# Kernel optimization log

Hardware: AMD Instinct MI355X
Metric: run time of the kernel (lower is better)

## Reference

```python
import jax, jax.numpy as jnp
import numpy as np
import math

D_MODEL, D_K, D_V, H = 512, 64, 64, 8

def setup_inputs() -> dict:
    key = jax.random.key(0)
    ks = jax.random.split(key, 8)
    B, L = 2, 4096
    q = jax.random.normal(ks[0], (B, L, D_MODEL), dtype=jnp.float32)
    k = jax.random.normal(ks[1], (B, L, D_MODEL), dtype=jnp.float32)
    v = jax.random.normal(ks[2], (B, L, D_MODEL), dtype=jnp.float32)
    attention_mask = jnp.ones((B, L), dtype=jnp.int32)
    s = 1.0 / math.sqrt(D_MODEL)
    Wq = jax.random.uniform(ks[3], (D_MODEL, H * D_K), dtype=jnp.float32, minval=-s, maxval=s)
    Wk = jax.random.uniform(ks[4], (D_MODEL, H * D_K), dtype=jnp.float32, minval=-s, maxval=s)
    Wv = jax.random.uniform(ks[5], (D_MODEL, H * D_V), dtype=jnp.float32, minval=-s, maxval=s)
    so = 1.0 / math.sqrt(H * D_V)
    Wo = jax.random.uniform(ks[6], (H * D_V, D_MODEL), dtype=jnp.float32, minval=-so, maxval=so)
    return {"q": q, "k": k, "v": v, "attention_mask": attention_mask,
            "Wq": Wq, "Wk": Wk, "Wv": Wv, "Wo": Wo}

def reference(q, k, v, attention_mask, Wq, Wk, Wv, Wo):
    B, L, _ = q.shape
    scale = 1.0 / math.sqrt(D_K)
    # project and split heads: [B, H, L, d]
    qh = (q @ Wq).reshape(B, L, H, D_K).transpose(0, 2, 1, 3)
    kh = (k @ Wk).reshape(B, L, H, D_K).transpose(0, 2, 1, 3)
    vh = (v @ Wv).reshape(B, L, H, D_V).transpose(0, 2, 1, 3)
    score = jnp.einsum('bhqd,bhkd->bhqk', qh, kh) * scale  # [B,H,L,L]
    mask = attention_mask[:, None, None, :]  # [B,1,1,L]
    score = jnp.where(mask == 0, -jnp.inf, score)
    attn = jax.nn.softmax(score, axis=-1)
    out = jnp.einsum('bhqk,bhkd->bhqd', attn, vh)
    out = out.transpose(0, 2, 1, 3).reshape(B, L, H * D_V)
    return out @ Wo
```

## Files before the change

### kernel.cpp

```cpp
#include <hip/hip_runtime.h>

typedef short bf16x8 __attribute__((ext_vector_type(8)));
typedef float f32x4 __attribute__((ext_vector_type(4)));
typedef unsigned short u16x8 __attribute__((ext_vector_type(8)));

static __device__ __forceinline__ unsigned short f2bf(float f) {
  unsigned int x = __builtin_bit_cast(unsigned int, f);
  x += 0x7FFFu + ((x >> 16) & 1u);
  return (unsigned short)(x >> 16);
}
static __device__ __forceinline__ unsigned int pk2bf(float a, float b) {
  unsigned int ia = __builtin_bit_cast(unsigned int, a) + 0x8000u;
  unsigned int ib = __builtin_bit_cast(unsigned int, b) + 0x8000u;
  return __builtin_amdgcn_perm(ib, ia, 0x07060302u);
}
static __device__ __forceinline__ void gl2lds16(const unsigned short* g, unsigned short* l) {
  __builtin_amdgcn_global_load_lds(
      (const __attribute__((address_space(1))) unsigned int*)g,
      (__attribute__((address_space(3))) unsigned int*)l, 16, 0, 0);
}

__global__ __launch_bounds__(256) void cvt3(const float* __restrict__ q, const float* __restrict__ k,
                                            const float* __restrict__ v,
                                            unsigned short* __restrict__ xbf) {
  const int sec = blockIdx.y;
  const float* src = (sec == 0) ? q : (sec == 1) ? k : v;
  int i = (blockIdx.x * 256 + threadIdx.x) * 8;
  int row = i >> 9, col = i & 511;
  float4 a = *(const float4*)(src + i);
  float4 b = *(const float4*)(src + i + 4);
  uint4 pk;
  pk.x = pk2bf(a.x, a.y); pk.y = pk2bf(a.z, a.w);
  pk.z = pk2bf(b.x, b.y); pk.w = pk2bf(b.z, b.w);
  *(uint4*)(xbf + (size_t)row * 1536 + sec * 512 + col) = pk;
}

__global__ __launch_bounds__(256) void wtrans4(const float* __restrict__ Wq, const float* __restrict__ Wk,
                                               const float* __restrict__ Wv, const float* __restrict__ Wo,
                                               unsigned short* __restrict__ WT) {
  __shared__ __align__(16) float T[64 * 68];
  const int z = blockIdx.z;
  const float* W = (z == 0) ? Wq : (z == 1) ? Wk : (z == 2) ? Wv : Wo;
  unsigned short* out = WT + (size_t)z * 512 * 512;
  const int k0 = blockIdx.x * 64, n0 = blockIdx.y * 64;
  const int tid = threadIdx.x;
#pragma unroll
  for (int i = 0; i < 4; ++i) {
    int chunk = i * 256 + tid;
    int row = chunk >> 4, fc = chunk & 15;
    *(float4*)(T + row * 68 + fc * 4) =
        *(const float4*)(W + (size_t)(k0 + row) * 512 + n0 + fc * 4);
  }
  __syncthreads();
#pragma unroll
  for (int i = 0; i < 2; ++i) {
    int chunk = i * 256 + tid;
    int nr = chunk >> 3, kc = chunk & 7;
    u16x8 v;
#pragma unroll
    for (int j = 0; j < 8; ++j) v[j] = f2bf(T[(kc * 8 + j) * 68 + nr]);
    *(u16x8*)(out + (size_t)(n0 + nr) * 512 + k0 + kc * 8) = v;
  }
}

__global__ __launch_bounds__(256) void gemm_qkv(const unsigned short* __restrict__ xbf,
                                                const unsigned short* __restrict__ Bt,
                                                unsigned short* __restrict__ C,
                                                float qscale) {
  __shared__ __align__(16) unsigned short Abuf[2][128 * 32];
  __shared__ __align__(16) unsigned short Bbuf[2][128 * 32];
  const int by = blockIdx.y;
  const unsigned short* A = xbf + (by >> 2) * 512;
  const float scale = (by < 4) ? qscale : 1.0f;
  const int tid = threadIdx.x;
  const int wid = tid >> 6, lane = tid & 63, quad = lane >> 4, li = lane & 15;
  const int bm = blockIdx.x * 128, bn = by * 128;
  const int wm = (wid & 1) * 64, wn = (wid >> 1) * 64;
  const unsigned short* ga[2]; int oa[2];
  const unsigned short* gb[2]; int obx[2];
#pragma unroll
  for (int i = 0; i < 2; ++i) {
    int lam = i * 256 + tid;
    int r = lam >> 2, c = (lam & 3) ^ (r & 3);
    ga[i] = A + (size_t)(bm + r) * 1536 + c * 8;
    oa[i] = lam * 8;
    gb[i] = Bt + (size_t)(bn + r) * 512 + c * 8;
    obx[i] = lam * 8;
  }
#pragma unroll
  for (int i = 0; i < 2; ++i) {
    gl2lds16(ga[i], &Abuf[0][oa[i]]); ga[i] += 32;
    gl2lds16(gb[i], &Bbuf[0][obx[i]]); gb[i] += 32;
  }
  f32x4 acc[4][4] = {};
  const int sw = li & 3;
  for (int s = 0; s < 16; ++s) {
    __syncthreads();
    if (s + 1 < 16) {
      int p = (s + 1) & 1;
#pragma unroll
      for (int i = 0; i < 2; ++i) {
        gl2lds16(ga[i], &Abuf[p][oa[i]]); ga[i] += 32;
        gl2lds16(gb[i], &Bbuf[p][obx[i]]); gb[i] += 32;
      }
    }
    const unsigned short* As = &Abuf[s & 1][0];
    const unsigned short* Bs = &Bbuf[s & 1][0];
    bf16x8 af[4], bfr[4];
#pragma unroll
    for (int t = 0; t < 4; ++t) {
      af[t]  = *(const bf16x8*)(As + (wm + t * 16 + li) * 32 + ((quad ^ sw) * 8));
      bfr[t] = *(const bf16x8*)(Bs + (wn + t * 16 + li) * 32 + ((quad ^ sw) * 8));
    }
#pragma unroll
    for (int mt = 0; mt < 4; ++mt)
#pragma unroll
      for (int nt = 0; nt < 4; ++nt)
        acc[mt][nt] = __builtin_amdgcn_mfma_f32_16x16x32_bf16(af[mt], bfr[nt], acc[mt][nt], 0, 0, 0);
  }
#pragma unroll
  for (int mt = 0; mt < 4; ++mt)
#pragma unroll
    for (int nt = 0; nt < 4; ++nt) {
      int r0 = bm + wm + mt * 16 + quad * 4;
      int c  = bn + wn + nt * 16 + li;
#pragma unroll
      for (int r = 0; r < 4; ++r)
        C[(size_t)(r0 + r) * 1536 + c] = f2bf(acc[mt][nt][r] * scale);
    }
}

__global__ __launch_bounds__(256) void gemm_o(const unsigned short* __restrict__ A,
                                              const unsigned short* __restrict__ Bt,
                                              float* __restrict__ Cf) {
  __shared__ __align__(16) unsigned short Abuf[2][128 * 64];
  __shared__ __align__(16) unsigned short Bbuf[2][64 * 64];
  const int K = 512, LDC = 512;
  const int tid = threadIdx.x;
  const int wid = tid >> 6, lane = tid & 63, quad = lane >> 4, li = lane & 15;
  const int bm = blockIdx.x * 128, bn = blockIdx.y * 64;
  const int wm = wid * 32;
  const unsigned short* ga[4]; int oa[4];
  const unsigned short* gb[2]; int ob[2];
#pragma unroll
  for (int i = 0; i < 4; ++i) {
    int lam = i * 256 + wid * 64 + lane;
    int r = lam >> 3, c = (lam & 7) ^ (r & 7);
    ga[i] = A + (size_t)(bm + r) * K + c * 8;
    oa[i] = lam * 8;
  }
#pragma unroll
  for (int i = 0; i < 2; ++i) {
    int lam = i * 256 + wid * 64 + lane;
    int r = lam >> 3, c = (lam & 7) ^ (r & 7);
    gb[i] = Bt + (size_t)(bn + r) * K + c * 8;
    ob[i] = lam * 8;
  }
#pragma unroll
  for (int i = 0; i < 4; ++i) { gl2lds16(ga[i], &Abuf[0][oa[i]]); ga[i] += 64; }
#pragma unroll
  for (int i = 0; i < 2; ++i) { gl2lds16(gb[i], &Bbuf[0][ob[i]]); gb[i] += 64; }

  f32x4 acc[2][4] = {};
  const int sw = li & 7;
  for (int s = 0; s < 8; ++s) {
    __syncthreads();
    if (s + 1 < 8) {
      int p = (s + 1) & 1;
#pragma unroll
      for (int i = 0; i < 4; ++i) { gl2lds16(ga[i], &Abuf[p][oa[i]]); ga[i] += 64; }
#pragma unroll
      for (int i = 0; i < 2; ++i) { gl2lds16(gb[i], &Bbuf[p][ob[i]]); gb[i] += 64; }
    }
    const unsigned short* As = &Abuf[s & 1][0];
    const unsigned short* Bs = &Bbuf[s & 1][0];
#pragma unroll
    for (int kk = 0; kk < 2; ++kk) {
      bf16x8 af[2], bfr[4];
#pragma unroll
      for (int t = 0; t < 2; ++t)
        af[t] = *(const bf16x8*)(As + (wm + t * 16 + li) * 64 + (((kk * 4 + quad) ^ sw) * 8));
#pragma unroll
      for (int t = 0; t < 4; ++t)
        bfr[t] = *(const bf16x8*)(Bs + (t * 16 + li) * 64 + (((kk * 4 + quad) ^ sw) * 8));
#pragma unroll
      for (int mt = 0; mt < 2; ++mt)
#pragma unroll
        for (int nt = 0; nt < 4; ++nt)
          acc[mt][nt] = __builtin_amdgcn_mfma_f32_16x16x32_bf16(af[mt], bfr[nt], acc[mt][nt], 0, 0, 0);
    }
  }
#pragma unroll
  for (int mt = 0; mt < 2; ++mt)
#pragma unroll
    for (int nt = 0; nt < 4; ++nt) {
      int r0 = bm + wm + mt * 16 + quad * 4;
      int c  = bn + nt * 16 + li;
#pragma unroll
      for (int r = 0; r < 4; ++r)
        Cf[(size_t)(r0 + r) * LDC + c] = acc[mt][nt][r];
    }
}

__global__ __launch_bounds__(256) void vtrans(const unsigned short* __restrict__ qkv,
                                              unsigned short* __restrict__ vt) {
  __shared__ __align__(16) unsigned short T[64 * 72];
  const int kt = blockIdx.x;
  const int bh = blockIdx.y;
  const int b = bh >> 3, h = bh & 7;
  const int tid = threadIdx.x;
#pragma unroll
  for (int i = 0; i < 2; ++i) {
    int chunk = i * 256 + tid;
    int row = chunk >> 3, c8 = chunk & 7;
    *(uint4*)(T + row * 72 + c8 * 8) =
        *(const uint4*)(qkv + (size_t)(b * 4096 + kt * 64 + row) * 1536 + 1024 + h * 64 + c8 * 8);
  }
  __syncthreads();
#pragma unroll
  for (int i = 0; i < 2; ++i) {
    int chunk = i * 256 + tid;
    int dr = chunk >> 3, c8 = chunk & 7;
    u16x8 v;
#pragma unroll
    for (int j = 0; j < 8; ++j) v[j] = T[(c8 * 8 + j) * 72 + dr];
    *(u16x8*)(vt + (size_t)(bh * 64 + dr) * 4096 + kt * 64 + c8 * 8) = v;
  }
}

__global__ __launch_bounds__(512) void attn(const unsigned short* __restrict__ qkv,
                                            const unsigned short* __restrict__ vt,
                                            const int* __restrict__ mask,
                                            float* __restrict__ O0, float* __restrict__ O1,
                                            float* __restrict__ Lb) {
  __shared__ __align__(16) unsigned short Kbuf[2][64 * 64];
  __shared__ __align__(16) unsigned short Vbuf[2][64 * 64];
  __shared__ __align__(16) unsigned short Psh[8][16 * 72];
  __shared__ __align__(16) unsigned short MskBits[256];
  const int qt = blockIdx.x, h = blockIdx.y, z = blockIdx.z;
  const int b = z >> 1, half = z & 1;
  const int t0 = half * 32;
  const int tid = threadIdx.x;
  const int wid = tid >> 6, lane = tid & 63, quad = lane >> 4, li = lane & 15;
  const size_t tok0 = (size_t)b * 4096;

  if (tid < 256) {
    const int4* mp = (const int4*)(mask + b * 4096 + tid * 16);
    unsigned int bits = 0;
#pragma unroll
    for (int j = 0; j < 4; ++j) {
      int4 m4 = mp[j];
      bits |= (m4.x ? 1u : 0u) << (j * 4 + 0);
      bits |= (m4.y ? 1u : 0u) << (j * 4 + 1);
      bits |= (m4.z ? 1u : 0u) << (j * 4 + 2);
      bits |= (m4.w ? 1u : 0u) << (j * 4 + 3);
    }
    MskBits[tid] = (unsigned short)bits;
  }

  const unsigned short* qp = qkv + (tok0 + qt * 128 + wid * 16 + li) * 1536 + h * 64;
  bf16x8 bq0 = *(const bf16x8*)(qp + quad * 8);
  bf16x8 bq1 = *(const bf16x8*)(qp + 32 + quad * 8);

  const unsigned short* kbase = qkv + tok0 * 1536 + 512 + h * 64;
  const unsigned short* vbase = vt + (size_t)(b * 8 + h) * 64 * 4096;
  const int wk = wid & 3;
  const int lam0 = wk * 128 + lane, lam1 = lam0 + 64;
  const int r0 = lam0 >> 3, c0 = (lam0 & 7) ^ (r0 & 7);
  const int r1 = lam1 >> 3, c1 = (lam1 & 7) ^ (r1 & 7);
  const unsigned short *g0, *g1;
  size_t kstride;
  unsigned short *lb0, *lb1;
  if (wid < 4) {
    g0 = kbase + (size_t)(t0 * 64 + r0) * 1536 + c0 * 8;
    g1 = kbase + (size_t)(t0 * 64 + r1) * 1536 + c1 * 8;
    kstride = (size_t)64 * 1536;
    lb0 = &Kbuf[0][0]; lb1 = &Kbuf[1][0];
  } else {
    g0 = vbase + (size_t)r0 * 4096 + t0 * 64 + c0 * 8;
    g1 = vbase + (size_t)r1 * 4096 + t0 * 64 + c1 * 8;
    kstride = 64;
    lb0 = &Vbuf[0][0]; lb1 = &Vbuf[1][0];
  }
  const int o0 = lam0 * 8, o1 = lam1 * 8;

  gl2lds16(g0, lb0 + o0);
  gl2lds16(g1, lb0 + o1);
  g0 += kstride; g1 += kstride;

  f32x4 accO[4] = {};
  f32x4 accL = {};
  bf16x8 bones;
#pragma unroll
  for (int j = 0; j < 8; ++j) bones[j] = (short)0x3F80;
  unsigned short* Pw = &Psh[wid][0];
  const int sw = li & 7;

  for (int tt = 0; tt < 32; ++tt) {
    const int t = t0 + tt;
    __syncthreads();
    if (tt < 31) {
      unsigned short* lb = ((tt + 1) & 1) ? lb1 : lb0;
      gl2lds16(g0, lb + o0);
      gl2lds16(g1, lb + o1);
      g0 += kstride; g1 += kstride;
    }
    const unsigned short* Ks = &Kbuf[tt & 1][0];
    const unsigned short* Vs = &Vbuf[tt & 1][0];

    f32x4 s[4];
#pragma unroll
    for (int kb = 0; kb < 4; ++kb) {
      const unsigned short* kr = Ks + (kb * 16 + li) * 64;
      bf16x8 ak0 = *(const bf16x8*)(kr + ((quad ^ sw) * 8));
      bf16x8 ak1 = *(const bf16x8*)(kr + (((4 + quad) ^ sw) * 8));
      f32x4 zv = {};
      zv = __builtin_amdgcn_mfma_f32_16x16x32_bf16(ak0, bq0, zv, 0, 0, 0);
      zv = __builtin_amdgcn_mfma_f32_16x16x32_bf16(ak1, bq1, zv, 0, 0, 0);
      s[kb] = zv;
    }
    unsigned long long mbits = *(const unsigned long long*)(MskBits + t * 4);
    if (mbits != ~0ull) {
#pragma unroll
      for (int kb = 0; kb < 4; ++kb)
#pragma unroll
        for (int r = 0; r < 4; ++r) {
          int key = kb * 16 + quad * 4 + r;
          if (!((mbits >> key) & 1ull)) s[kb][r] = -1e30f;
        }
    }
#pragma unroll
    for (int kb = 0; kb < 4; ++kb) {
#pragma unroll
      for (int r = 0; r < 4; ++r) s[kb][r] = __builtin_amdgcn_exp2f(s[kb][r]);
      uint2 pk;
      pk.x = pk2bf(s[kb][0], s[kb][1]);
      pk.y = pk2bf(s[kb][2], s[kb][3]);
      *(uint2*)(Pw + li * 72 + kb * 16 + quad * 4) = pk;
    }
    bf16x8 p0 = *(const bf16x8*)(Pw + li * 72 + quad * 8);
    bf16x8 p1 = *(const bf16x8*)(Pw + li * 72 + 32 + quad * 8);
#pragma unroll
    for (int dc = 0; dc < 4; ++dc) {
      const unsigned short* vr = Vs + (dc * 16 + li) * 64;
      bf16x8 bv0 = *(const bf16x8*)(vr + ((quad ^ sw) * 8));
      bf16x8 bv1 = *(const bf16x8*)(vr + (((4 + quad) ^ sw) * 8));
      accO[dc] = __builtin_amdgcn_mfma_f32_16x16x32_bf16(p0, bv0, accO[dc], 0, 0, 0);
      accO[dc] = __builtin_amdgcn_mfma_f32_16x16x32_bf16(p1, bv1, accO[dc], 0, 0, 0);
    }
    accL = __builtin_amdgcn_mfma_f32_16x16x32_bf16(p0, bones, accL, 0, 0, 0);
    accL = __builtin_amdgcn_mfma_f32_16x16x32_bf16(p1, bones, accL, 0, 0, 0);
  }
  float* Oh = half ? O1 : O0;
  const size_t rq = tok0 + qt * 128 + wid * 16 + quad * 4;
#pragma unroll
  for (int dc = 0; dc < 4; ++dc) {
    size_t col = h * 64 + dc * 16 + li;
#pragma unroll
    for (int r = 0; r < 4; ++r)
      Oh[(rq + r) * 512 + col] = accO[dc][r];
  }
  if (li == 0) {
#pragma unroll
    for (int r = 0; r < 4; ++r)
      Lb[((size_t)half * 8192 + rq + r) * 8 + h] = accL[r];
  }
}

__global__ __launch_bounds__(256) void cmb(const float* __restrict__ O0, const float* __restrict__ O1,
                                           const float* __restrict__ Lb,
                                           unsigned short* __restrict__ ob) {
  int idx = (blockIdx.x * 256 + threadIdx.x) * 4;
  int tok = idx >> 9, h = (idx >> 6) & 7;
  float inv = 1.f / (Lb[(size_t)tok * 8 + h] + Lb[(size_t)(8192 + tok) * 8 + h]);
  float4 a = *(const float4*)(O0 + idx);
  float4 b = *(const float4*)(O1 + idx);
  uint2 pk;
  pk.x = pk2bf((a.x + b.x) * inv, (a.y + b.y) * inv);
  pk.y = pk2bf((a.z + b.z) * inv, (a.w + b.w) * inv);
  *(uint2*)(ob + idx) = pk;
}

extern "C" void kernel_launch(void* const* d_in, const int* in_sizes, int n_in,
                              void* d_out, int out_size, void* d_ws, size_t ws_size,
                              hipStream_t stream) {
  const float* q  = (const float*)d_in[0];
  const float* k  = (const float*)d_in[1];
  const float* v  = (const float*)d_in[2];
  const int* mask = (const int*)d_in[3];
  const float* Wq = (const float*)d_in[4];
  const float* Wk = (const float*)d_in[5];
  const float* Wv = (const float*)d_in[6];
  const float* Wo = (const float*)d_in[7];
  float* out = (float*)d_out;

  char* ws = (char*)d_ws;
  const size_t MB = 1024 * 1024;
  unsigned short* xbf  = (unsigned short*)(ws);
  unsigned short* vtb  = (unsigned short*)(ws + 16 * MB);
  unsigned short* obb  = (unsigned short*)(ws + 16 * MB);
  unsigned short* qkvh = (unsigned short*)(ws + 24 * MB);
  unsigned short* wAll = (unsigned short*)(ws + 48 * MB);
  unsigned short* woT  = wAll + (size_t)3 * 512 * 512;
  float* O0f = (float*)(ws);
  float* O1f = (float*)(ws + 50 * MB);
  float* Lb  = (float*)(ws + 66 * MB);

  dim3 cg(2048, 3);
  cvt3<<<cg, 256, 0, stream>>>(q, k, v, xbf);
  dim3 wg(8, 8, 4);
  wtrans4<<<wg, 256, 0, stream>>>(Wq, Wk, Wv, Wo, wAll);
  const float qscale = 0.125f * 1.44269504f;
  dim3 gq(64, 12);
  gemm_qkv<<<gq, 256, 0, stream>>>(xbf, wAll, qkvh, qscale);
  dim3 vg(64, 16);
  vtrans<<<vg, 256, 0, stream>>>(qkvh, vtb);
  dim3 ag(32, 8, 4);
  attn<<<ag, 512, 0, stream>>>(qkvh, vtb, mask, O0f, O1f, Lb);
  cmb<<<4096, 256, 0, stream>>>(O0f, O1f, Lb, obb);
  dim3 go(64, 8);
  gemm_o<<<go, 256, 0, stream>>>(obb, woT, out);
}
```

Baseline: 235.1 us.

## Fuse input conversion into QKV GEMM, combine into O GEMM, widen attention waves

Removes the separate fp32-to-bf16 conversion kernel by having the QKV GEMM load fp32 inputs through registers, convert them and store to LDS with software prefetch. Removes the split-combine kernel by folding normalization and the two-half sum into the output GEMM's A-tile load. Attention now uses 256 threads with each wave handling 32 query rows, so K/V tiles in LDS are reused across two MFMA row groups. Grid axes are swapped so blocks sharing the same A rows run adjacently. This trades async global-to-LDS loads for register-staged loads and more VGPR pressure in exchange for fewer launches and less intermediate memory traffic.

Result: slower. 287.7 us (+22.4%).

```diff
diff --git a/kernel.cpp b/kernel.cpp
--- a/kernel.cpp
+++ b/kernel.cpp
@@ -14,25 +14,16 @@
   unsigned int ib = __builtin_bit_cast(unsigned int, b) + 0x8000u;
   return __builtin_amdgcn_perm(ib, ia, 0x07060302u);
 }
+static __device__ __forceinline__ uint4 pk8bf(float4 a, float4 b) {
+  uint4 r;
+  r.x = pk2bf(a.x, a.y); r.y = pk2bf(a.z, a.w);
+  r.z = pk2bf(b.x, b.y); r.w = pk2bf(b.z, b.w);
+  return r;
+}
 static __device__ __forceinline__ void gl2lds16(const unsigned short* g, unsigned short* l) {
   __builtin_amdgcn_global_load_lds(
       (const __attribute__((address_space(1))) unsigned int*)g,
       (__attribute__((address_space(3))) unsigned int*)l, 16, 0, 0);
-}
-
-__global__ __launch_bounds__(256) void cvt3(const float* __restrict__ q, const float* __restrict__ k,
-                                            const float* __restrict__ v,
-                                            unsigned short* __restrict__ xbf) {
-  const int sec = blockIdx.y;
-  const float* src = (sec == 0) ? q : (sec == 1) ? k : v;
-  int i = (blockIdx.x * 256 + threadIdx.x) * 8;
-  int row = i >> 9, col = i & 511;
-  float4 a = *(const float4*)(src + i);
-  float4 b = *(const float4*)(src + i + 4);
-  uint4 pk;
-  pk.x = pk2bf(a.x, a.y); pk.y = pk2bf(a.z, a.w);
-  pk.z = pk2bf(b.x, b.y); pk.w = pk2bf(b.z, b.w);
-  *(uint4*)(xbf + (size_t)row * 1536 + sec * 512 + col) = pk;
 }
 
 __global__ __launch_bounds__(256) void wtrans4(const float* __restrict__ Wq, const float* __restrict__ Wk,
@@ -63,45 +54,61 @@
   }
 }
 
-__global__ __launch_bounds__(256) void gemm_qkv(const unsigned short* __restrict__ xbf,
+__global__ __launch_bounds__(256) void gemm_qkv(const float* __restrict__ Aq, const float* __restrict__ Ak,
+                                                const float* __restrict__ Av,
                                                 const unsigned short* __restrict__ Bt,
-                                                unsigned short* __restrict__ C,
-                                                float qscale) {
+                                                unsigned short* __restrict__ C, float qscale) {
   __shared__ __align__(16) unsigned short Abuf[2][128 * 32];
   __shared__ __align__(16) unsigned short Bbuf[2][128 * 32];
-  const int by = blockIdx.y;
-  const unsigned short* A = xbf + (by >> 2) * 512;
+  const int by = blockIdx.x;
+  const float* A = (by < 4) ? Aq : (by < 8) ? Ak : Av;
   const float scale = (by < 4) ? qscale : 1.0f;
   const int tid = threadIdx.x;
   const int wid = tid >> 6, lane = tid & 63, quad = lane >> 4, li = lane & 15;
-  const int bm = blockIdx.x * 128, bn = by * 128;
+  const int bm = blockIdx.y * 128, bn = by * 128;
   const int wm = (wid & 1) * 64, wn = (wid >> 1) * 64;
-  const unsigned short* ga[2]; int oa[2];
   const unsigned short* gb[2]; int obx[2];
 #pragma unroll
   for (int i = 0; i < 2; ++i) {
     int lam = i * 256 + tid;
-    int r = lam >> 2, c = (lam & 3) ^ (r & 3);
-    ga[i] = A + (size_t)(bm + r) * 1536 + c * 8;
-    oa[i] = lam * 8;
-    gb[i] = Bt + (size_t)(bn + r) * 512 + c * 8;
+    int r = lam >> 2, cc = (lam & 3) ^ (r & 3);
+    gb[i] = Bt + (size_t)(bn + r) * 512 + cc * 8;
     obx[i] = lam * 8;
   }
-#pragma unroll
-  for (int i = 0; i < 2; ++i) {
-    gl2lds16(ga[i], &Abuf[0][oa[i]]); ga[i] += 32;
-    gl2lds16(gb[i], &Bbuf[0][obx[i]]); gb[i] += 32;
-  }
+  int ar[2], ac[2], ao[2];
+#pragma unroll
+  for (int i = 0; i < 2; ++i) {
+    int c = i * 256 + tid;
+    ar[i] = c >> 2;
+    ac[i] = ((c & 3) ^ (ar[i] & 3)) * 8;
+    ao[i] = c * 8;
+  }
+  float4 av0[2], av1[2];
+#pragma unroll
+  for (int i = 0; i < 2; ++i) {
+    const float* ap = A + (size_t)(bm + ar[i]) * 512 + ac[i];
+    av0[i] = *(const float4*)ap;
+    av1[i] = *(const float4*)(ap + 4);
+  }
+#pragma unroll
+  for (int i = 0; i < 2; ++i) *(uint4*)(&Abuf[0][ao[i]]) = pk8bf(av0[i], av1[i]);
+#pragma unroll
+  for (int i = 0; i < 2; ++i) { gl2lds16(gb[i], &Bbuf[0][obx[i]]); gb[i] += 32; }
+
   f32x4 acc[4][4] = {};
   const int sw = li & 3;
   for (int s = 0; s < 16; ++s) {
     __syncthreads();
-    if (s + 1 < 16) {
-      int p = (s + 1) & 1;
+    const bool pf = (s + 1 < 16);
+    const int p = (s + 1) & 1;
+    if (pf) {
+#pragma unroll
+      for (int i = 0; i < 2; ++i) { gl2lds16(gb[i], &Bbuf[p][obx[i]]); gb[i] += 32; }
 #pragma unroll
       for (int i = 0; i < 2; ++i) {
-        gl2lds16(ga[i], &Abuf[p][oa[i]]); ga[i] += 32;
-        gl2lds16(gb[i], &Bbuf[p][obx[i]]); gb[i] += 32;
+        const float* ap = A + (size_t)(bm + ar[i]) * 512 + (s + 1) * 32 + ac[i];
+        av0[i] = *(const float4*)ap;
+        av1[i] = *(const float4*)(ap + 4);
       }
     }
     const unsigned short* As = &Abuf[s & 1][0];
@@ -117,6 +124,10 @@
 #pragma unroll
       for (int nt = 0; nt < 4; ++nt)
         acc[mt][nt] = __builtin_amdgcn_mfma_f32_16x16x32_bf16(af[mt], bfr[nt], acc[mt][nt], 0, 0, 0);
+    if (pf) {
+#pragma unroll
+      for (int i = 0; i < 2; ++i) *(uint4*)(&Abuf[p][ao[i]]) = pk8bf(av0[i], av1[i]);
+    }
   }
 #pragma unroll
   for (int mt = 0; mt < 4; ++mt)
@@ -127,78 +138,6 @@
 #pragma unroll
       for (int r = 0; r < 4; ++r)
         C[(size_t)(r0 + r) * 1536 + c] = f2bf(acc[mt][nt][r] * scale);
-    }
-}
-
-__global__ __launch_bounds__(256) void gemm_o(const unsigned short* __restrict__ A,
-                                              const unsigned short* __restrict__ Bt,
-                                              float* __restrict__ Cf) {
-  __shared__ __align__(16) unsigned short Abuf[2][128 * 64];
-  __shared__ __align__(16) unsigned short Bbuf[2][64 * 64];
-  const int K = 512, LDC = 512;
-  const int tid = threadIdx.x;
-  const int wid = tid >> 6, lane = tid & 63, quad = lane >> 4, li = lane & 15;
-  const int bm = blockIdx.x * 128, bn = blockIdx.y * 64;
-  const int wm = wid * 32;
-  const unsigned short* ga[4]; int oa[4];
-  const unsigned short* gb[2]; int ob[2];
-#pragma unroll
-  for (int i = 0; i < 4; ++i) {
-    int lam = i * 256 + wid * 64 + lane;
-    int r = lam >> 3, c = (lam & 7) ^ (r & 7);
-    ga[i] = A + (size_t)(bm + r) * K + c * 8;
-    oa[i] = lam * 8;
-  }
-#pragma unroll
-  for (int i = 0; i < 2; ++i) {
-    int lam = i * 256 + wid * 64 + lane;
-    int r = lam >> 3, c = (lam & 7) ^ (r & 7);
-    gb[i] = Bt + (size_t)(bn + r) * K + c * 8;
-    ob[i] = lam * 8;
-  }
-#pragma unroll
-  for (int i = 0; i < 4; ++i) { gl2lds16(ga[i], &Abuf[0][oa[i]]); ga[i] += 64; }
-#pragma unroll
-  for (int i = 0; i < 2; ++i) { gl2lds16(gb[i], &Bbuf[0][ob[i]]); gb[i] += 64; }
-
-  f32x4 acc[2][4] = {};
-  const int sw = li & 7;
-  for (int s = 0; s < 8; ++s) {
-    __syncthreads();
-    if (s + 1 < 8) {
-      int p = (s + 1) & 1;
-#pragma unroll
-      for (int i = 0; i < 4; ++i) { gl2lds16(ga[i], &Abuf[p][oa[i]]); ga[i] += 64; }
-#pragma unroll
-      for (int i = 0; i < 2; ++i) { gl2lds16(gb[i], &Bbuf[p][ob[i]]); gb[i] += 64; }
-    }
-    const unsigned short* As = &Abuf[s & 1][0];
-    const unsigned short* Bs = &Bbuf[s & 1][0];
-#pragma unroll
-    for (int kk = 0; kk < 2; ++kk) {
-      bf16x8 af[2], bfr[4];
-#pragma unroll
-      for (int t = 0; t < 2; ++t)
-        af[t] = *(const bf16x8*)(As + (wm + t * 16 + li) * 64 + (((kk * 4 + quad) ^ sw) * 8));
-#pragma unroll
-      for (int t = 0; t < 4; ++t)
-        bfr[t] = *(const bf16x8*)(Bs + (t * 16 + li) * 64 + (((kk * 4 + quad) ^ sw) * 8));
-#pragma unroll
-      for (int mt = 0; mt < 2; ++mt)
-#pragma unroll
-        for (int nt = 0; nt < 4; ++nt)
-          acc[mt][nt] = __builtin_amdgcn_mfma_f32_16x16x32_bf16(af[mt], bfr[nt], acc[mt][nt], 0, 0, 0);
-    }
-  }
-#pragma unroll
-  for (int mt = 0; mt < 2; ++mt)
-#pragma unroll
-    for (int nt = 0; nt < 4; ++nt) {
-      int r0 = bm + wm + mt * 16 + quad * 4;
-      int c  = bn + nt * 16 + li;
-#pragma unroll
-      for (int r = 0; r < 4; ++r)
-        Cf[(size_t)(r0 + r) * LDC + c] = acc[mt][nt][r];
     }
 }
 
@@ -228,14 +167,14 @@
   }
 }
 
-__global__ __launch_bounds__(512) void attn(const unsigned short* __restrict__ qkv,
+__global__ __launch_bounds__(256) void attn(const unsigned short* __restrict__ qkv,
                                             const unsigned short* __restrict__ vt,
                                             const int* __restrict__ mask,
                                             float* __restrict__ O0, float* __restrict__ O1,
                                             float* __restrict__ Lb) {
   __shared__ __align__(16) unsigned short Kbuf[2][64 * 64];
   __shared__ __align__(16) unsigned short Vbuf[2][64 * 64];
-  __shared__ __align__(16) unsigned short Psh[8][16 * 72];
+  __shared__ __align__(16) unsigned short Psh[4][32 * 72];
   __shared__ __align__(16) unsigned short MskBits[256];
   const int qt = blockIdx.x, h = blockIdx.y, z = blockIdx.z;
   const int b = z >> 1, half = z & 1;
@@ -244,7 +183,7 @@
   const int wid = tid >> 6, lane = tid & 63, quad = lane >> 4, li = lane & 15;
   const size_t tok0 = (size_t)b * 4096;
 
-  if (tid < 256) {
+  {
     const int4* mp = (const int4*)(mask + b * 4096 + tid * 16);
     unsigned int bits = 0;
 #pragma unroll
@@ -258,38 +197,34 @@
     MskBits[tid] = (unsigned short)bits;
   }
 
-  const unsigned short* qp = qkv + (tok0 + qt * 128 + wid * 16 + li) * 1536 + h * 64;
-  bf16x8 bq0 = *(const bf16x8*)(qp + quad * 8);
-  bf16x8 bq1 = *(const bf16x8*)(qp + 32 + quad * 8);
+  const unsigned short* qpa = qkv + (tok0 + qt * 128 + wid * 32 + li) * 1536 + h * 64;
+  const unsigned short* qpb = qpa + 16 * 1536;
+  bf16x8 bq0a = *(const bf16x8*)(qpa + quad * 8);
+  bf16x8 bq1a = *(const bf16x8*)(qpa + 32 + quad * 8);
+  bf16x8 bq0b = *(const bf16x8*)(qpb + quad * 8);
+  bf16x8 bq1b = *(const bf16x8*)(qpb + 32 + quad * 8);
 
   const unsigned short* kbase = qkv + tok0 * 1536 + 512 + h * 64;
   const unsigned short* vbase = vt + (size_t)(b * 8 + h) * 64 * 4096;
-  const int wk = wid & 3;
-  const int lam0 = wk * 128 + lane, lam1 = lam0 + 64;
-  const int r0 = lam0 >> 3, c0 = (lam0 & 7) ^ (r0 & 7);
-  const int r1 = lam1 >> 3, c1 = (lam1 & 7) ^ (r1 & 7);
-  const unsigned short *g0, *g1;
-  size_t kstride;
-  unsigned short *lb0, *lb1;
-  if (wid < 4) {
-    g0 = kbase + (size_t)(t0 * 64 + r0) * 1536 + c0 * 8;
-    g1 = kbase + (size_t)(t0 * 64 + r1) * 1536 + c1 * 8;
-    kstride = (size_t)64 * 1536;
-    lb0 = &Kbuf[0][0]; lb1 = &Kbuf[1][0];
-  } else {
-    g0 = vbase + (size_t)r0 * 4096 + t0 * 64 + c0 * 8;
-    g1 = vbase + (size_t)r1 * 4096 + t0 * 64 + c1 * 8;
-    kstride = 64;
-    lb0 = &Vbuf[0][0]; lb1 = &Vbuf[1][0];
-  }
-  const int o0 = lam0 * 8, o1 = lam1 * 8;
-
-  gl2lds16(g0, lb0 + o0);
-  gl2lds16(g1, lb0 + o1);
-  g0 += kstride; g1 += kstride;
-
-  f32x4 accO[4] = {};
-  f32x4 accL = {};
+  const unsigned short *gk[2], *gv[2];
+  int okc[2], ovc[2];
+#pragma unroll
+  for (int i = 0; i < 2; ++i) {
+    int c = i * 256 + tid;
+    int r = c >> 3, cc = (c & 7) ^ (r & 7);
+    gk[i] = kbase + (size_t)(t0 * 64 + r) * 1536 + cc * 8;
+    gv[i] = vbase + (size_t)r * 4096 + t0 * 64 + cc * 8;
+    okc[i] = c * 8;
+    ovc[i] = c * 8;
+  }
+#pragma unroll
+  for (int i = 0; i < 2; ++i) {
+    gl2lds16(gk[i], &Kbuf[0][okc[i]]); gk[i] += (size_t)64 * 1536;
+    gl2lds16(gv[i], &Vbuf[0][ovc[i]]); gv[i] += 64;
+  }
+
+  f32x4 accOa[4] = {}, accOb[4] = {};
+  f32x4 accLa = {}, accLb = {};
   bf16x8 bones;
 #pragma unroll
   for (int j = 0; j < 8; ++j) bones[j] = (short)0x3F80;
@@ -300,24 +235,28 @@
     const int t = t0 + tt;
     __syncthreads();
     if (tt < 31) {
-      unsigned short* lb = ((tt + 1) & 1) ? lb1 : lb0;
-      gl2lds16(g0, lb + o0);
-      gl2lds16(g1, lb + o1);
-      g0 += kstride; g1 += kstride;
+      const int p = (tt + 1) & 1;
+#pragma unroll
+      for (int i = 0; i < 2; ++i) {
+        gl2lds16(gk[i], &Kbuf[p][okc[i]]); gk[i] += (size_t)64 * 1536;
+        gl2lds16(gv[i], &Vbuf[p][ovc[i]]); gv[i] += 64;
+      }
     }
     const unsigned short* Ks = &Kbuf[tt & 1][0];
     const unsigned short* Vs = &Vbuf[tt & 1][0];
 
-    f32x4 s[4];
+    f32x4 sa[4], sb[4];
 #pragma unroll
     for (int kb = 0; kb < 4; ++kb) {
       const unsigned short* kr = Ks + (kb * 16 + li) * 64;
       bf16x8 ak0 = *(const bf16x8*)(kr + ((quad ^ sw) * 8));
       bf16x8 ak1 = *(const bf16x8*)(kr + (((4 + quad) ^ sw) * 8));
-      f32x4 zv = {};
-      zv = __builtin_amdgcn_mfma_f32_16x16x32_bf16(ak0, bq0, zv, 0, 0, 0);
-      zv = __builtin_amdgcn_mfma_f32_16x16x32_bf16(ak1, bq1, zv, 0, 0, 0);
-      s[kb] = zv;
+      f32x4 za = {}, zb = {};
+      za = __builtin_amdgcn_mfma_f32_16x16x32_bf16(ak0, bq0a, za, 0, 0, 0);
+      za = __builtin_amdgcn_mfma_f32_16x16x32_bf16(ak1, bq1a, za, 0, 0, 0);
+      zb = __builtin_amdgcn_mfma_f32_16x16x32_bf16(ak0, bq0b, zb, 0, 0, 0);
+      zb = __builtin_amdgcn_mfma_f32_16x16x32_bf16(ak1, bq1b, zb, 0, 0, 0);
+      sa[kb] = za; sb[kb] = zb;
     }
     unsigned long long mbits = *(const unsigned long long*)(MskBits + t * 4);
     if (mbits != ~0ull) {
@@ -326,59 +265,166 @@
 #pragma unroll
         for (int r = 0; r < 4; ++r) {
           int key = kb * 16 + quad * 4 + r;
-          if (!((mbits >> key) & 1ull)) s[kb][r] = -1e30f;
+          if (!((mbits >> key) & 1ull)) { sa[kb][r] = -1e30f; sb[kb][r] = -1e30f; }
         }
     }
 #pragma unroll
     for (int kb = 0; kb < 4; ++kb) {
 #pragma unroll
-      for (int r = 0; r < 4; ++r) s[kb][r] = __builtin_amdgcn_exp2f(s[kb][r]);
-      uint2 pk;
-      pk.x = pk2bf(s[kb][0], s[kb][1]);
-      pk.y = pk2bf(s[kb][2], s[kb][3]);
-      *(uint2*)(Pw + li * 72 + kb * 16 + quad * 4) = pk;
-    }
-    bf16x8 p0 = *(const bf16x8*)(Pw + li * 72 + quad * 8);
-    bf16x8 p1 = *(const bf16x8*)(Pw + li * 72 + 32 + quad * 8);
+      for (int r = 0; r < 4; ++r) {
+        sa[kb][r] = __builtin_amdgcn_exp2f(sa[kb][r]);
+        sb[kb][r] = __builtin_amdgcn_exp2f(sb[kb][r]);
+      }
+      uint2 pka, pkb;
+      pka.x = pk2bf(sa[kb][0], sa[kb][1]); pka.y = pk2bf(sa[kb][2], sa[kb][3]);
+      pkb.x = pk2bf(sb[kb][0], sb[kb][1]); pkb.y = pk2bf(sb[kb][2], sb[kb][3]);
+      *(uint2*)(Pw + li * 72 + kb * 16 + quad * 4) = pka;
+      *(uint2*)(Pw + (li + 16) * 72 + kb * 16 + quad * 4) = pkb;
+    }
+    bf16x8 p0a = *(const bf16x8*)(Pw + li * 72 + quad * 8);
+    bf16x8 p1a = *(const bf16x8*)(Pw + li * 72 + 32 + quad * 8);
+    bf16x8 p0b = *(const bf16x8*)(Pw + (li + 16) * 72 + quad * 8);
+    bf16x8 p1b = *(const bf16x8*)(Pw + (li + 16) * 72 + 32 + quad * 8);
 #pragma unroll
     for (int dc = 0; dc < 4; ++dc) {
       const unsigned short* vr = Vs + (dc * 16 + li) * 64;
       bf16x8 bv0 = *(const bf16x8*)(vr + ((quad ^ sw) * 8));
       bf16x8 bv1 = *(const bf16x8*)(vr + (((4 + quad) ^ sw) * 8));
-      accO[dc] = __builtin_amdgcn_mfma_f32_16x16x32_bf16(p0, bv0, accO[dc], 0, 0, 0);
-      accO[dc] = __builtin_amdgcn_mfma_f32_16x16x32_bf16(p1, bv1, accO[dc], 0, 0, 0);
-    }
-    accL = __builtin_amdgcn_mfma_f32_16x16x32_bf16(p0, bones, accL, 0, 0, 0);
-    accL = __builtin_amdgcn_mfma_f32_16x16x32_bf16(p1, bones, accL, 0, 0, 0);
+      accOa[dc] = __builtin_amdgcn_mfma_f32_16x16x32_bf16(p0a, bv0, accOa[dc], 0, 0, 0);
+      accOa[dc] = __builtin_amdgcn_mfma_f32_16x16x32_bf16(p1a, bv1, accOa[dc], 0, 0, 0);
+      accOb[dc] = __builtin_amdgcn_mfma_f32_16x16x32_bf16(p0b, bv0, accOb[dc], 0, 0, 0);
+      accOb[dc] = __builtin_amdgcn_mfma_f32_16x16x32_bf16(p1b, bv1, accOb[dc], 0, 0, 0);
+    }
+    accLa = __builtin_amdgcn_mfma_f32_16x16x32_bf16(p0a, bones, accLa, 0, 0, 0);
+    accLa = __builtin_amdgcn_mfma_f32_16x16x32_bf16(p1a, bones, accLa, 0, 0, 0);
+    accLb = __builtin_amdgcn_mfma_f32_16x16x32_bf16(p0b, bones, accLb, 0, 0, 0);
+    accLb = __builtin_amdgcn_mfma_f32_16x16x32_bf16(p1b, bones, accLb, 0, 0, 0);
   }
   float* Oh = half ? O1 : O0;
-  const size_t rq = tok0 + qt * 128 + wid * 16 + quad * 4;
+  const size_t rqa = tok0 + qt * 128 + wid * 32 + quad * 4;
+  const size_t rqb = rqa + 16;
 #pragma unroll
   for (int dc = 0; dc < 4; ++dc) {
     size_t col = h * 64 + dc * 16 + li;
 #pragma unroll
-    for (int r = 0; r < 4; ++r)
-      Oh[(rq + r) * 512 + col] = accO[dc][r];
+    for (int r = 0; r < 4; ++r) {
+      Oh[(rqa + r) * 512 + col] = accOa[dc][r];
+      Oh[(rqb + r) * 512 + col] = accOb[dc][r];
+    }
   }
   if (li == 0) {
 #pragma unroll
-    for (int r = 0; r < 4; ++r)
-      Lb[((size_t)half * 8192 + rq + r) * 8 + h] = accL[r];
-  }
-}
-
-__global__ __launch_bounds__(256) void cmb(const float* __restrict__ O0, const float* __restrict__ O1,
-                                           const float* __restrict__ Lb,
-                                           unsigned short* __restrict__ ob) {
-  int idx = (blockIdx.x * 256 + threadIdx.x) * 4;
-  int tok = idx >> 9, h = (idx >> 6) & 7;
-  float inv = 1.f / (Lb[(size_t)tok * 8 + h] + Lb[(size_t)(8192 + tok) * 8 + h]);
-  float4 a = *(const float4*)(O0 + idx);
-  float4 b = *(const float4*)(O1 + idx);
-  uint2 pk;
-  pk.x = pk2bf((a.x + b.x) * inv, (a.y + b.y) * inv);
-  pk.y = pk2bf((a.z + b.z) * inv, (a.w + b.w) * inv);
-  *(uint2*)(ob + idx) = pk;
+    for (int r = 0; r < 4; ++r) {
+      Lb[((size_t)half * 8192 + rqa + r) * 8 + h] = accLa[r];
+      Lb[((size_t)half * 8192 + rqb + r) * 8 + h] = accLb[r];
+    }
+  }
+}
+
+__global__ __launch_bounds__(256) void gemm_o(const float* __restrict__ O0, const float* __restrict__ O1,
+                                              const float* __restrict__ Lb,
+                                              const unsigned short* __restrict__ Bt,
+                                              float* __restrict__ Cf) {
+  __shared__ __align__(16) unsigned short Abuf[2][128 * 64];
+  __shared__ __align__(16) unsigned short Bbuf[2][64 * 64];
+  const int tid = threadIdx.x;
+  const int wid = tid >> 6, lane = tid & 63, quad = lane >> 4, li = lane & 15;
+  const int bm = blockIdx.y * 128, bn = blockIdx.x * 64;
+  const int wm = wid * 32;
+  const unsigned short* gb[2]; int obx[2];
+#pragma unroll
+  for (int i = 0; i < 2; ++i) {
+    int lam = i * 256 + tid;
+    int r = lam >> 3, cc = (lam & 7) ^ (r & 7);
+    gb[i] = Bt + (size_t)(bn + r) * 512 + cc * 8;
+    obx[i] = lam * 8;
+  }
+  int ar[4], ac[4], ao[4];
+#pragma unroll
+  for (int i = 0; i < 4; ++i) {
+    int c = i * 256 + tid;
+    ar[i] = c >> 3;
+    ac[i] = ((c & 7) ^ (ar[i] & 7)) * 8;
+    ao[i] = c * 8;
+  }
+  uint4 apk[4];
+#pragma unroll
+  for (int i = 0; i < 4; ++i) {
+    size_t tok = bm + ar[i];
+    float inv = 1.f / (Lb[tok * 8 + 0] + Lb[(8192 + tok) * 8 + 0]);
+    const float* p0 = O0 + tok * 512 + ac[i];
+    const float* p1 = O1 + tok * 512 + ac[i];
+    float4 a0 = *(const float4*)p0, a1 = *(const float4*)(p0 + 4);
+    float4 b0 = *(const float4*)p1, b1 = *(const float4*)(p1 + 4);
+    float4 c0, c1;
+    c0.x = (a0.x + b0.x) * inv; c0.y = (a0.y + b0.y) * inv;
+    c0.z = (a0.z + b0.z) * inv; c0.w = (a0.w + b0.w) * inv;
+    c1.x = (a1.x + b1.x) * inv; c1.y = (a1.y + b1.y) * inv;
+    c1.z = (a1.z + b1.z) * inv; c1.w = (a1.w + b1.w) * inv;
+    apk[i] = pk8bf(c0, c1);
+  }
+#pragma unroll
+  for (int i = 0; i < 4; ++i) *(uint4*)(&Abuf[0][ao[i]]) = apk[i];
+#pragma unroll
+  for (int i = 0; i < 2; ++i) { gl2lds16(gb[i], &Bbuf[0][obx[i]]); gb[i] += 64; }
+
+  f32x4 acc[2][4] = {};
+  const int sw = li & 7;
+  for (int s = 0; s < 8; ++s) {
+    __syncthreads();
+    const bool pf = (s + 1 < 8);
+    const int p = (s + 1) & 1;
+    if (pf) {
+#pragma unroll
+      for (int i = 0; i < 2; ++i) { gl2lds16(gb[i], &Bbuf[p][obx[i]]); gb[i] += 64; }
+#pragma unroll
+      for (int i = 0; i < 4; ++i) {
+        size_t tok = bm + ar[i];
+        float inv = 1.f / (Lb[tok * 8 + (s + 1)] + Lb[(8192 + tok) * 8 + (s + 1)]);
+        const float* p0 = O0 + tok * 512 + (s + 1) * 64 + ac[i];
+        const float* p1 = O1 + tok * 512 + (s + 1) * 64 + ac[i];
+        float4 a0 = *(const float4*)p0, a1 = *(const float4*)(p0 + 4);
+        float4 b0 = *(const float4*)p1, b1 = *(const float4*)(p1 + 4);
+        float4 c0, c1;
+        c0.x = (a0.x + b0.x) * inv; c0.y = (a0.y + b0.y) * inv;
+        c0.z = (a0.z + b0.z) * inv; c0.w = (a0.w + b0.w) * inv;
+        c1.x = (a1.x + b1.x) * inv; c1.y = (a1.y + b1.y) * inv;
+        c1.z = (a1.z + b1.z) * inv; c1.w = (a1.w + b1.w) * inv;
+        apk[i] = pk8bf(c0, c1);
+      }
+    }
+    const unsigned short* As = &Abuf[s & 1][0];
+    const unsigned short* Bs = &Bbuf[s & 1][0];
+#pragma unroll
+    for (int kk = 0; kk < 2; ++kk) {
+      bf16x8 af[2], bfr[4];
+#pragma unroll
+      for (int t = 0; t < 2; ++t)
+        af[t] = *(const bf16x8*)(As + (wm + t * 16 + li) * 64 + (((kk * 4 + quad) ^ sw) * 8));
+#pragma unroll
+      for (int t = 0; t < 4; ++t)
+        bfr[t] = *(const bf16x8*)(Bs + (t * 16 + li) * 64 + (((kk * 4 + quad) ^ sw) * 8));
+#pragma unroll
+      for (int mt = 0; mt < 2; ++mt)
+#pragma unroll
+        for (int nt = 0; nt < 4; ++nt)
+          acc[mt][nt] = __builtin_amdgcn_mfma_f32_16x16x32_bf16(af[mt], bfr[nt], acc[mt][nt], 0, 0, 0);
+    }
+    if (pf) {
+#pragma unroll
+      for (int i = 0; i < 4; ++i) *(uint4*)(&Abuf[p][ao[i]]) = apk[i];
+    }
+  }
+#pragma unroll
+  for (int mt = 0; mt < 2; ++mt)
+#pragma unroll
+    for (int nt = 0; nt < 4; ++nt) {
+      int r0 = bm + wm + mt * 16 + quad * 4;
+      int c  = bn + nt * 16 + li;
+#pragma unroll
+      for (int r = 0; r < 4; ++r)
+        Cf[(size_t)(r0 + r) * 512 + c] = acc[mt][nt][r];
+    }
 }
 
 extern "C" void kernel_launch(void* const* d_in, const int* in_sizes, int n_in,
@@ -396,28 +442,23 @@
 
   char* ws = (char*)d_ws;
   const size_t MB = 1024 * 1024;
-  unsigned short* xbf  = (unsigned short*)(ws);
-  unsigned short* vtb  = (unsigned short*)(ws + 16 * MB);
-  unsigned short* obb  = (unsigned short*)(ws + 16 * MB);
-  unsigned short* qkvh = (unsigned short*)(ws + 24 * MB);
-  unsigned short* wAll = (unsigned short*)(ws + 48 * MB);
+  unsigned short* qkvh = (unsigned short*)(ws);
+  unsigned short* vtb  = (unsigned short*)(ws + 24 * MB);
+  float* O0f = (float*)(ws + 32 * MB);
+  float* O1f = (float*)(ws + 48 * MB);
+  float* Lb  = (float*)(ws + 64 * MB);
+  unsigned short* wAll = (unsigned short*)(ws + 65 * MB);
   unsigned short* woT  = wAll + (size_t)3 * 512 * 512;
-  float* O0f = (float*)(ws);
-  float* O1f = (float*)(ws + 50 * MB);
-  float* Lb  = (float*)(ws + 66 * MB);
-
-  dim3 cg(2048, 3);
-  cvt3<<<cg, 256, 0, stream>>>(q, k, v, xbf);
+
   dim3 wg(8, 8, 4);
   wtrans4<<<wg, 256, 0, stream>>>(Wq, Wk, Wv, Wo, wAll);
   const float qscale = 0.125f * 1.44269504f;
-  dim3 gq(64, 12);
-  gemm_qkv<<<gq, 256, 0, stream>>>(xbf, wAll, qkvh, qscale);
+  dim3 gq(12, 64);
+  gemm_qkv<<<gq, 256, 0, stream>>>(q, k, v, wAll, qkvh, qscale);
   dim3 vg(64, 16);
   vtrans<<<vg, 256, 0, stream>>>(qkvh, vtb);
   dim3 ag(32, 8, 4);
-  attn<<<ag, 512, 0, stream>>>(qkvh, vtb, mask, O0f, O1f, Lb);
-  cmb<<<4096, 256, 0, stream>>>(O0f, O1f, Lb, obb);
-  dim3 go(64, 8);
-  gemm_o<<<go, 256, 0, stream>>>(obb, woT, out);
-}
+  attn<<<ag, 256, 0, stream>>>(qkvh, vtb, mask, O0f, O1f, Lb);
+  dim3 go(8, 64);
+  gemm_o<<<go, 256, 0, stream>>>(O0f, O1f, Lb, woT, out);
+}
```

## Process 32 query rows per wave in attention to reuse K/V tiles

Applied to the files above, without the earlier changes.

Each wave in the attention kernel now handles two 16-row query sub-tiles instead of one. Each block covers 256 queries and the grid along the query axis is halved. K and V fragments read from LDS are reused across both sub-tiles, which halves global K/V traffic and LDS fragment reads per query. The cost is more accumulator registers and a larger P scratch buffer in shared memory, which may lower occupancy. The grid drops to 512 blocks, which on a 256-CU device can leave load imbalance.

Measured after the change: 232.4 us. About the same (-1.2%).

```diff
diff --git a/kernel.cpp b/kernel.cpp
--- a/kernel.cpp
+++ b/kernel.cpp
@@ -235,7 +235,7 @@
                                             float* __restrict__ Lb) {
   __shared__ __align__(16) unsigned short Kbuf[2][64 * 64];
   __shared__ __align__(16) unsigned short Vbuf[2][64 * 64];
-  __shared__ __align__(16) unsigned short Psh[8][16 * 72];
+  __shared__ __align__(16) unsigned short Psh[8][32 * 72];
   __shared__ __align__(16) unsigned short MskBits[256];
   const int qt = blockIdx.x, h = blockIdx.y, z = blockIdx.z;
   const int b = z >> 1, half = z & 1;
@@ -258,9 +258,12 @@
     MskBits[tid] = (unsigned short)bits;
   }
 
-  const unsigned short* qp = qkv + (tok0 + qt * 128 + wid * 16 + li) * 1536 + h * 64;
-  bf16x8 bq0 = *(const bf16x8*)(qp + quad * 8);
-  bf16x8 bq1 = *(const bf16x8*)(qp + 32 + quad * 8);
+  const unsigned short* qpa = qkv + (tok0 + qt * 256 + wid * 32 + li) * 1536 + h * 64;
+  const unsigned short* qpb = qpa + 16 * 1536;
+  bf16x8 bq0a = *(const bf16x8*)(qpa + quad * 8);
+  bf16x8 bq1a = *(const bf16x8*)(qpa + 32 + quad * 8);
+  bf16x8 bq0b = *(const bf16x8*)(qpb + quad * 8);
+  bf16x8 bq1b = *(const bf16x8*)(qpb + 32 + quad * 8);
 
   const unsigned short* kbase = qkv + tok0 * 1536 + 512 + h * 64;
   const unsigned short* vbase = vt + (size_t)(b * 8 + h) * 64 * 4096;
@@ -288,8 +291,8 @@
   gl2lds16(g1, lb0 + o1);
   g0 += kstride; g1 += kstride;
 
-  f32x4 accO[4] = {};
-  f32x4 accL = {};
+  f32x4 accOa[4] = {}, accOb[4] = {};
+  f32x4 accLa = {}, accLb = {};
   bf16x8 bones;
 #pragma unroll
   for (int j = 0; j < 8; ++j) bones[j] = (short)0x3F80;
@@ -308,16 +311,18 @@
     const unsigned short* Ks = &Kbuf[tt & 1][0];
     const unsigned short* Vs = &Vbuf[tt & 1][0];
 
-    f32x4 s[4];
+    f32x4 sa[4], sb[4];
 #pragma unroll
     for (int kb = 0; kb < 4; ++kb) {
       const unsigned short* kr = Ks + (kb * 16 + li) * 64;
       bf16x8 ak0 = *(const bf16x8*)(kr + ((quad ^ sw) * 8));
       bf16x8 ak1 = *(const bf16x8*)(kr + (((4 + quad) ^ sw) * 8));
-      f32x4 zv = {};
-      zv = __builtin_amdgcn_mfma_f32_16x16x32_bf16(ak0, bq0, zv, 0, 0, 0);
-      zv = __builtin_amdgcn_mfma_f32_16x16x32_bf16(ak1, bq1, zv, 0, 0, 0);
-      s[kb] = zv;
+      f32x4 za = {}, zb = {};
+      za = __builtin_amdgcn_mfma_f32_16x16x32_bf16(ak0, bq0a, za, 0, 0, 0);
+      za = __builtin_amdgcn_mfma_f32_16x16x32_bf16(ak1, bq1a, za, 0, 0, 0);
+      zb = __builtin_amdgcn_mfma_f32_16x16x32_bf16(ak0, bq0b, zb, 0, 0, 0);
+      zb = __builtin_amdgcn_mfma_f32_16x16x32_bf16(ak1, bq1b, zb, 0, 0, 0);
+      sa[kb] = za; sb[kb] = zb;
     }
     unsigned long long mbits = *(const unsigned long long*)(MskBits + t * 4);
     if (mbits != ~0ull) {
@@ -326,44 +331,59 @@
 #pragma unroll
         for (int r = 0; r < 4; ++r) {
           int key = kb * 16 + quad * 4 + r;
-          if (!((mbits >> key) & 1ull)) s[kb][r] = -1e30f;
+          if (!((mbits >> key) & 1ull)) { sa[kb][r] = -1e30f; sb[kb][r] = -1e30f; }
         }
     }
 #pragma unroll
     for (int kb = 0; kb < 4; ++kb) {
 #pragma unroll
-      for (int r = 0; r < 4; ++r) s[kb][r] = __builtin_amdgcn_exp2f(s[kb][r]);
-      uint2 pk;
-      pk.x = pk2bf(s[kb][0], s[kb][1]);
-      pk.y = pk2bf(s[kb][2], s[kb][3]);
-      *(uint2*)(Pw + li * 72 + kb * 16 + quad * 4) = pk;
-    }
-    bf16x8 p0 = *(const bf16x8*)(Pw + li * 72 + quad * 8);
-    bf16x8 p1 = *(const bf16x8*)(Pw + li * 72 + 32 + quad * 8);
+      for (int r = 0; r < 4; ++r) {
+        sa[kb][r] = __builtin_amdgcn_exp2f(sa[kb][r]);
+        sb[kb][r] = __builtin_amdgcn_exp2f(sb[kb][r]);
+      }
+      uint2 pka, pkb;
+      pka.x = pk2bf(sa[kb][0], sa[kb][1]); pka.y = pk2bf(sa[kb][2], sa[kb][3]);
+      pkb.x = pk2bf(sb[kb][0], sb[kb][1]); pkb.y = pk2bf(sb[kb][2], sb[kb][3]);
+      *(uint2*)(Pw + li * 72 + kb * 16 + quad * 4) = pka;
+      *(uint2*)(Pw + (li + 16) * 72 + kb * 16 + quad * 4) = pkb;
+    }
+    bf16x8 p0a = *(const bf16x8*)(Pw + li * 72 + quad * 8);
+    bf16x8 p1a = *(const bf16x8*)(Pw + li * 72 + 32 + quad * 8);
+    bf16x8 p0b = *(const bf16x8*)(Pw + (li + 16) * 72 + quad * 8);
+    bf16x8 p1b = *(const bf16x8*)(Pw + (li + 16) * 72 + 32 + quad * 8);
 #pragma unroll
     for (int dc = 0; dc < 4; ++dc) {
       const unsigned short* vr = Vs + (dc * 16 + li) * 64;
       bf16x8 bv0 = *(const bf16x8*)(vr + ((quad ^ sw) * 8));
       bf16x8 bv1 = *(const bf16x8*)(vr + (((4 + quad) ^ sw) * 8));
-      accO[dc] = __builtin_amdgcn_mfma_f32_16x16x32_bf16(p0, bv0, accO[dc], 0, 0, 0);
-      accO[dc] = __builtin_amdgcn_mfma_f32_16x16x32_bf16(p1, bv1, accO[dc], 0, 0, 0);
-    }
-    accL = __builtin_amdgcn_mfma_f32_16x16x32_bf16(p0, bones, accL, 0, 0, 0);
-    accL = __builtin_amdgcn_mfma_f32_16x16x32_bf16(p1, bones, accL, 0, 0, 0);
+      accOa[dc] = __builtin_amdgcn_mfma_f32_16x16x32_bf16(p0a, bv0, accOa[dc], 0, 0, 0);
+      accOa[dc] = __builtin_amdgcn_mfma_f32_16x16x32_bf16(p1a, bv1, accOa[dc], 0, 0, 0);
+      accOb[dc] = __builtin_amdgcn_mfma_f32_16x16x32_bf16(p0b, bv0, accOb[dc], 0, 0, 0);
+      accOb[dc] = __builtin_amdgcn_mfma_f32_16x16x32_bf16(p1b, bv1, accOb[dc], 0, 0, 0);
+    }
+    accLa = __builtin_amdgcn_mfma_f32_16x16x32_bf16(p0a, bones, accLa, 0, 0, 0);
+    accLa = __builtin_amdgcn_mfma_f32_16x16x32_bf16(p1a, bones, accLa, 0, 0, 0);
+    accLb = __builtin_amdgcn_mfma_f32_16x16x32_bf16(p0b, bones, accLb, 0, 0, 0);
+    accLb = __builtin_amdgcn_mfma_f32_16x16x32_bf16(p1b, bones, accLb, 0, 0, 0);
   }
   float* Oh = half ? O1 : O0;
-  const size_t rq = tok0 + qt * 128 + wid * 16 + quad * 4;
+  const size_t rqa = tok0 + qt * 256 + wid * 32 + quad * 4;
+  const size_t rqb = rqa + 16;
 #pragma unroll
   for (int dc = 0; dc < 4; ++dc) {
     size_t col = h * 64 + dc * 16 + li;
 #pragma unroll
-    for (int r = 0; r < 4; ++r)
-      Oh[(rq + r) * 512 + col] = accO[dc][r];
+    for (int r = 0; r < 4; ++r) {
+      Oh[(rqa + r) * 512 + col] = accOa[dc][r];
+      Oh[(rqb + r) * 512 + col] = accOb[dc][r];
+    }
   }
   if (li == 0) {
 #pragma unroll
-    for (int r = 0; r < 4; ++r)
-      Lb[((size_t)half * 8192 + rq + r) * 8 + h] = accL[r];
+    for (int r = 0; r < 4; ++r) {
+      Lb[((size_t)half * 8192 + rqa + r) * 8 + h] = accLa[r];
+      Lb[((size_t)half * 8192 + rqb + r) * 8 + h] = accLb[r];
+    }
   }
 }
 
@@ -415,7 +435,7 @@
   gemm_qkv<<<gq, 256, 0, stream>>>(xbf, wAll, qkvh, qscale);
   dim3 vg(64, 16);
   vtrans<<<vg, 256, 0, stream>>>(qkvh, vtb);
-  dim3 ag(32, 8, 4);
+  dim3 ag(16, 8, 4);
   attn<<<ag, 512, 0, stream>>>(qkvh, vtb, mask, O0f, O1f, Lb);
   cmb<<<4096, 256, 0, stream>>>(O0f, O1f, Lb, obb);
   dim3 go(64, 8);
```
